# Optimization experiments

Measured on AMD Instinct MI355X. Metric: run time of the kernel, lower is better.

## Reference

```python
import jax, jax.numpy as jnp
import numpy as np
import math

N_FREQS = 32
MARGIN = 0.1
CHOUT = 270
POS_DIM = 2 * N_FREQS ** 2  # 2048


def fourier_emb(positions):
    # positions: [..., 2] in [0, 1]
    width = 1.0 + 2.0 * MARGIN
    p = (positions + MARGIN) / width
    f = jnp.arange(N_FREQS, dtype=p.dtype)
    two_pi = 2.0 * math.pi
    # phase[..., i, j] = 2*pi*(x*i + y*j)  -> flatten to [..., F*F]
    phase = two_pi * (p[..., 0][..., None, None] * f[:, None]
                      + p[..., 1][..., None, None] * f[None, :])
    phase = phase.reshape(*phase.shape[:-2], N_FREQS * N_FREQS)
    return jnp.concatenate([jnp.sin(phase), jnp.cos(phase)], axis=-1)  # [..., 2F^2]


def setup_inputs() -> dict:
    key = jax.random.key(0)
    k1, k2, k3 = jax.random.split(key, 3)
    B, C, T = 32, 273, 3000
    brain_data = jax.random.normal(k1, (B, C, T), dtype=jnp.float32)
    channel_layout = jax.random.uniform(k2, (B, C, 2), dtype=jnp.float32)
    heads = jax.random.normal(k3, (CHOUT, POS_DIM), dtype=jnp.float32) / POS_DIM ** 0.5
    return {"brain_data": brain_data, "channel_layout": channel_layout, "heads": heads}


def reference(brain_data, channel_layout, heads):
    # Eval mode: all channels valid, no dropout mask, zero score offset.
    emb = fourier_emb(channel_layout)                      # [B, C, D]
    scores = jnp.einsum('bcd,od->boc', emb, heads)         # [B, O, C]
    weights = jax.nn.softmax(scores, axis=-1)              # softmax over channels
    out = jnp.einsum('bct,boc->bot', brain_data, weights)  # [B, O, T]
    return out
```

## Files before the change

### kernel.cpp

```cpp
#include <hip/hip_runtime.h>
#include <hip/hip_bf16.h>
#include <hip/hip_fp16.h>

#define NB 32
#define NC 273
#define NT 3000
#define NO 270
#define ND 2048
#define CP 288

typedef _Float16 f16x8 __attribute__((ext_vector_type(8)));
typedef float f32x4 __attribute__((ext_vector_type(4)));

#define S_OFF 55296000UL
#define W_OFF 64730880UL
#define H_OFF 69707520UL

__device__ __forceinline__ unsigned short f2h_bits(float f) {
  _Float16 h = (_Float16)f;
  unsigned short u;
  __builtin_memcpy(&u, &h, 2);
  return u;
}

__global__ void heads_cvt_kernel(const float* __restrict__ heads,
                                 _Float16* __restrict__ hh) {
  const size_t idx = ((size_t)blockIdx.x * 256 + threadIdx.x) * 8;
  const float4 a = *reinterpret_cast<const float4*>(heads + idx);
  const float4 c = *reinterpret_cast<const float4*>(heads + idx + 4);
  f16x8 v;
  v[0] = (_Float16)a.x; v[1] = (_Float16)a.y; v[2] = (_Float16)a.z; v[3] = (_Float16)a.w;
  v[4] = (_Float16)c.x; v[5] = (_Float16)c.y; v[6] = (_Float16)c.z; v[7] = (_Float16)c.w;
  *reinterpret_cast<f16x8*>(hh + idx) = v;
}

__global__ void emb_kernel(const float* __restrict__ layout,
                           _Float16* __restrict__ emb) {
  const int bc = blockIdx.x;
  const float x = layout[2 * bc];
  const float y = layout[2 * bc + 1];
  const float inv = 1.0f / 1.2f;
  const float px = (x + 0.1f) * inv;
  const float py = (y + 0.1f) * inv;
  const float two_pi = 6.283185307179586f;

  const int d0 = threadIdx.x * 8;
  const bool is_sin = d0 < 1024;
  const int dd0 = d0 & 1023;
  const int i = dd0 >> 5;
  const int j = dd0 & 31;
  const float base = px * (float)i + py * (float)j;

  unsigned short h[8];
#pragma unroll
  for (int s = 0; s < 8; ++s) {
    const float ph = two_pi * (base + py * (float)s);
    const float v = is_sin ? sinf(ph) : cosf(ph);
    h[s] = f2h_bits(v);
  }
  uint4 u;
  u.x = (unsigned)h[0] | ((unsigned)h[1] << 16);
  u.y = (unsigned)h[2] | ((unsigned)h[3] << 16);
  u.z = (unsigned)h[4] | ((unsigned)h[5] << 16);
  u.w = (unsigned)h[6] | ((unsigned)h[7] << 16);
  *reinterpret_cast<uint4*>(emb + (size_t)bc * ND + d0) = u;
}

__global__ void scores_kernel(const _Float16* __restrict__ hh,
                              const _Float16* __restrict__ emb,
                              float* __restrict__ scores) {
  __shared__ _Float16 As[64][72];
  __shared__ _Float16 Bs[64][72];
  const int b = blockIdx.z, o0 = blockIdx.y * 64, c0 = blockIdx.x * 64;
  const int tid = threadIdx.x;
  const int lane = tid & 63, w = tid >> 6;
  const int wm = (w >> 1) * 32, wn = (w & 1) * 32;
  const int ln = lane & 15, quad = lane >> 4;
  const int sr = tid >> 2;
  const int sk = (tid & 3) * 16;
  const _Float16* embB = emb + (size_t)b * NC * ND;

  f32x4 acc[2][2] = {};

  for (int k0 = 0; k0 < ND; k0 += 64) {
    {
      const int o = o0 + sr;
      uint4 u0 = {0, 0, 0, 0}, u1 = {0, 0, 0, 0};
      if (o < NO) {
        const uint4* p = reinterpret_cast<const uint4*>(hh + (size_t)o * ND + k0 + sk);
        u0 = p[0]; u1 = p[1];
      }
      *reinterpret_cast<uint4*>(&As[sr][sk]) = u0;
      *reinterpret_cast<uint4*>(&As[sr][sk + 8]) = u1;
    }
    {
      const int c = c0 + sr;
      uint4 u0 = {0, 0, 0, 0}, u1 = {0, 0, 0, 0};
      if (c < NC) {
        const uint4* p = reinterpret_cast<const uint4*>(embB + (size_t)c * ND + k0 + sk);
        u0 = p[0]; u1 = p[1];
      }
      *reinterpret_cast<uint4*>(&Bs[sr][sk]) = u0;
      *reinterpret_cast<uint4*>(&Bs[sr][sk + 8]) = u1;
    }
    __syncthreads();
#pragma unroll
    for (int ks = 0; ks < 64; ks += 32) {
      const int kf = ks + quad * 8;
      const f16x8 a0 = *reinterpret_cast<const f16x8*>(&As[wm + ln][kf]);
      const f16x8 a1 = *reinterpret_cast<const f16x8*>(&As[wm + 16 + ln][kf]);
      const f16x8 b0 = *reinterpret_cast<const f16x8*>(&Bs[wn + ln][kf]);
      const f16x8 b1 = *reinterpret_cast<const f16x8*>(&Bs[wn + 16 + ln][kf]);
      acc[0][0] = __builtin_amdgcn_mfma_f32_16x16x32_f16(a0, b0, acc[0][0], 0, 0, 0);
      acc[0][1] = __builtin_amdgcn_mfma_f32_16x16x32_f16(a0, b1, acc[0][1], 0, 0, 0);
      acc[1][0] = __builtin_amdgcn_mfma_f32_16x16x32_f16(a1, b0, acc[1][0], 0, 0, 0);
      acc[1][1] = __builtin_amdgcn_mfma_f32_16x16x32_f16(a1, b1, acc[1][1], 0, 0, 0);
    }
    __syncthreads();
  }

  float* sB = scores + (size_t)b * NO * NC;
#pragma unroll
  for (int i = 0; i < 2; ++i) {
    const int ob = o0 + wm + 16 * i + quad * 4;
#pragma unroll
    for (int j = 0; j < 2; ++j) {
      const int c = c0 + wn + 16 * j + ln;
      if (c >= NC) continue;
#pragma unroll
      for (int r = 0; r < 4; ++r) {
        const int o = ob + r;
        if (o < NO) sB[(size_t)o * NC + c] = acc[i][j][r];
      }
    }
  }
}

__global__ void softmax_kernel(const float* __restrict__ sc,
                               _Float16* __restrict__ wq) {
  const int row = blockIdx.x * 4 + (threadIdx.x >> 6);
  const int lane = threadIdx.x & 63;
  const float* p = sc + (size_t)row * NC;
  _Float16* q = wq + (size_t)row * CP;
  float v[5];
  float m = -3.0e38f;
#pragma unroll
  for (int k = 0; k < 5; ++k) {
    const int c = lane + k * 64;
    v[k] = (c < NC) ? p[c] : -3.0e38f;
    m = fmaxf(m, v[k]);
  }
#pragma unroll
  for (int off = 32; off > 0; off >>= 1) m = fmaxf(m, __shfl_xor(m, off));
  float s = 0.f;
#pragma unroll
  for (int k = 0; k < 5; ++k) {
    v[k] = expf(v[k] - m);
    s += v[k];
  }
#pragma unroll
  for (int off = 32; off > 0; off >>= 1) s += __shfl_xor(s, off);
  const float r = 1.0f / s;
#pragma unroll
  for (int k = 0; k < 5; ++k) {
    const int c = lane + k * 64;
    if (c < NC) q[c] = (_Float16)(v[k] * r);
    else if (c < CP) q[c] = (_Float16)0.f;
  }
}

__global__ void transpose_kernel(const float* __restrict__ brain,
                                 _Float16* __restrict__ xh) {
  __shared__ float tile[32][33];
  const int b = blockIdx.z;
  const int c0 = blockIdx.y * 32;
  const int t0 = blockIdx.x * 32;
  const int tid = threadIdx.x;
  {
    const int cl = tid >> 3, tl = (tid & 7) * 4;
    const int c = c0 + cl;
    float4 v = {0.f, 0.f, 0.f, 0.f};
    if (c < NC) {
      const int t = t0 + tl;
      const float* p = brain + ((size_t)b * NC + c) * NT + t;
      if (t + 3 < NT) {
        v = *reinterpret_cast<const float4*>(p);
      } else {
        if (t + 0 < NT) v.x = p[0];
        if (t + 1 < NT) v.y = p[1];
        if (t + 2 < NT) v.z = p[2];
        if (t + 3 < NT) v.w = p[3];
      }
    }
    tile[cl][tl + 0] = v.x;
    tile[cl][tl + 1] = v.y;
    tile[cl][tl + 2] = v.z;
    tile[cl][tl + 3] = v.w;
  }
  __syncthreads();
  {
    const int tl = tid >> 3, cl = (tid & 7) * 4;
    const int t = t0 + tl;
    if (t < NT) {
      const unsigned short h0 = f2h_bits(tile[cl + 0][tl]);
      const unsigned short h1 = f2h_bits(tile[cl + 1][tl]);
      const unsigned short h2 = f2h_bits(tile[cl + 2][tl]);
      const unsigned short h3 = f2h_bits(tile[cl + 3][tl]);
      uint2 u;
      u.x = (unsigned)h0 | ((unsigned)h1 << 16);
      u.y = (unsigned)h2 | ((unsigned)h3 << 16);
      *reinterpret_cast<uint2*>(xh + ((size_t)b * NT + t) * CP + c0 + cl) = u;
    }
  }
}

__global__ void out_kernel(const _Float16* __restrict__ wq,
                           const _Float16* __restrict__ xh,
                           float* __restrict__ out) {
  __shared__ _Float16 As[64][40];
  __shared__ _Float16 Bs[128][40];
  const int b = blockIdx.z, o0 = blockIdx.y * 64, t0 = blockIdx.x * 128;
  const int tid = threadIdx.x;
  const int lane = tid & 63, w = tid >> 6;
  const int wm = (w >> 1) * 32, wn = (w & 1) * 64;
  const int ln = lane & 15, quad = lane >> 4;
  const _Float16* Wb = wq + (size_t)b * NO * CP;
  const _Float16* Xb = xh + (size_t)b * NT * CP;

  const int ar = tid >> 2, ak = (tid & 3) * 8;
  const int br = tid >> 1, bk = (tid & 1) * 16;

  f32x4 acc[2][4] = {};

  for (int k0 = 0; k0 < CP; k0 += 32) {
    {
      const int o = o0 + ar;
      uint4 u = {0, 0, 0, 0};
      if (o < NO) u = *reinterpret_cast<const uint4*>(Wb + (size_t)o * CP + k0 + ak);
      *reinterpret_cast<uint4*>(&As[ar][ak]) = u;
    }
    {
      const int t = t0 + br;
      uint4 u0 = {0, 0, 0, 0}, u1 = {0, 0, 0, 0};
      if (t < NT) {
        const uint4* p = reinterpret_cast<const uint4*>(Xb + (size_t)t * CP + k0 + bk);
        u0 = p[0]; u1 = p[1];
      }
      *reinterpret_cast<uint4*>(&Bs[br][bk]) = u0;
      *reinterpret_cast<uint4*>(&Bs[br][bk + 8]) = u1;
    }
    __syncthreads();
    {
      const int kf = quad * 8;
      const f16x8 a0 = *reinterpret_cast<const f16x8*>(&As[wm + ln][kf]);
      const f16x8 a1 = *reinterpret_cast<const f16x8*>(&As[wm + 16 + ln][kf]);
#pragma unroll
      for (int j = 0; j < 4; ++j) {
        const f16x8 bj = *reinterpret_cast<const f16x8*>(&Bs[wn + 16 * j + ln][kf]);
        acc[0][j] = __builtin_amdgcn_mfma_f32_16x16x32_f16(a0, bj, acc[0][j], 0, 0, 0);
        acc[1][j] = __builtin_amdgcn_mfma_f32_16x16x32_f16(a1, bj, acc[1][j], 0, 0, 0);
      }
    }
    __syncthreads();
  }

  float* oB = out + (size_t)b * NO * NT;
#pragma unroll
  for (int i = 0; i < 2; ++i) {
    const int ob = o0 + wm + 16 * i + quad * 4;
#pragma unroll
    for (int j = 0; j < 4; ++j) {
      const int t = t0 + wn + 16 * j + ln;
      if (t >= NT) continue;
#pragma unroll
      for (int r = 0; r < 4; ++r) {
        const int o = ob + r;
        if (o < NO) oB[(size_t)o * NT + t] = acc[i][j][r];
      }
    }
  }
}

extern "C" void kernel_launch(void* const* d_in, const int* in_sizes, int n_in,
                              void* d_out, int out_size, void* d_ws, size_t ws_size,
                              hipStream_t stream) {
  const float* brain = (const float*)d_in[0];
  const float* layout = (const float*)d_in[1];
  const float* heads = (const float*)d_in[2];
  for (int i = 0; i < n_in; ++i) {
    if (in_sizes[i] == NB * NC * NT) brain = (const float*)d_in[i];
    else if (in_sizes[i] == NB * NC * 2) layout = (const float*)d_in[i];
    else if (in_sizes[i] == NO * ND) heads = (const float*)d_in[i];
  }
  float* out = (float*)d_out;

  _Float16* emb = (_Float16*)d_ws;
  _Float16* xh = (_Float16*)d_ws;
  float* scores = (float*)((char*)d_ws + S_OFF);
  _Float16* wq = (_Float16*)((char*)d_ws + W_OFF);
  _Float16* hh = (_Float16*)((char*)d_ws + H_OFF);

  heads_cvt_kernel<<<NO, 256, 0, stream>>>(heads, hh);
  emb_kernel<<<NB * NC, 256, 0, stream>>>(layout, emb);
  scores_kernel<<<dim3(5, 5, NB), 256, 0, stream>>>(hh, emb, scores);
  softmax_kernel<<<(NB * NO) / 4, 256, 0, stream>>>(scores, wq);
  transpose_kernel<<<dim3((NT + 31) / 32, CP / 32, NB), 256, 0, stream>>>(brain, xh);
  out_kernel<<<dim3((NT + 127) / 128, 5, NB), 256, 0, stream>>>(wq, xh, out);
}
```

Baseline: 309.2 us.

## Fuse Fourier embedding into scores GEMM and co-schedule with transpose in one launch

Removes the separate embedding kernel: the scores GEMM now builds the sin/cos Fourier tile in shared memory on the fly, using range-reduced phases and the hardware sin instruction, with cos expressed as a quarter-period shift. The scores GEMM and the brain-data transpose/fp16 conversion are merged into one launch, with blocks split by index, so the small GEMM grid can overlap with the bandwidth-bound transpose. The transpose tile is enlarged to 64x64 with wider vector loads and stores. This avoids writing and re-reading the large fp16 embedding buffer and two launches. In exchange, sin is recomputed for each output-row tile, and the hardware sin may be less accurate.

```diff
diff --git a/kernel.cpp b/kernel.cpp
--- a/kernel.cpp
+++ b/kernel.cpp
@@ -34,103 +34,163 @@
   *reinterpret_cast<f16x8*>(hh + idx) = v;
 }
 
-__global__ void emb_kernel(const float* __restrict__ layout,
-                           _Float16* __restrict__ emb) {
-  const int bc = blockIdx.x;
-  const float x = layout[2 * bc];
-  const float y = layout[2 * bc + 1];
-  const float inv = 1.0f / 1.2f;
-  const float px = (x + 0.1f) * inv;
-  const float py = (y + 0.1f) * inv;
-  const float two_pi = 6.283185307179586f;
-
-  const int d0 = threadIdx.x * 8;
-  const bool is_sin = d0 < 1024;
-  const int dd0 = d0 & 1023;
-  const int i = dd0 >> 5;
-  const int j = dd0 & 31;
-  const float base = px * (float)i + py * (float)j;
-
-  unsigned short h[8];
-#pragma unroll
-  for (int s = 0; s < 8; ++s) {
-    const float ph = two_pi * (base + py * (float)s);
-    const float v = is_sin ? sinf(ph) : cosf(ph);
-    h[s] = f2h_bits(v);
-  }
-  uint4 u;
-  u.x = (unsigned)h[0] | ((unsigned)h[1] << 16);
-  u.y = (unsigned)h[2] | ((unsigned)h[3] << 16);
-  u.z = (unsigned)h[4] | ((unsigned)h[5] << 16);
-  u.w = (unsigned)h[6] | ((unsigned)h[7] << 16);
-  *reinterpret_cast<uint4*>(emb + (size_t)bc * ND + d0) = u;
-}
-
-__global__ void scores_kernel(const _Float16* __restrict__ hh,
-                              const _Float16* __restrict__ emb,
-                              float* __restrict__ scores) {
-  __shared__ _Float16 As[64][72];
-  __shared__ _Float16 Bs[64][72];
-  const int b = blockIdx.z, o0 = blockIdx.y * 64, c0 = blockIdx.x * 64;
+#define SC_BLOCKS 800
+#define TR_TX 47
+#define TR_BLOCKS (TR_TX * 5 * NB)
+
+__global__ void mid_kernel(const _Float16* __restrict__ hh,
+                           const float* __restrict__ layout,
+                           const float* __restrict__ brain,
+                           float* __restrict__ scores,
+                           _Float16* __restrict__ xh) {
+  __shared__ __align__(16) char smem[18432];
+  const int gid = blockIdx.x;
   const int tid = threadIdx.x;
-  const int lane = tid & 63, w = tid >> 6;
-  const int wm = (w >> 1) * 32, wn = (w & 1) * 32;
-  const int ln = lane & 15, quad = lane >> 4;
-  const int sr = tid >> 2;
-  const int sk = (tid & 3) * 16;
-  const _Float16* embB = emb + (size_t)b * NC * ND;
-
-  f32x4 acc[2][2] = {};
-
-  for (int k0 = 0; k0 < ND; k0 += 64) {
-    {
-      const int o = o0 + sr;
-      uint4 u0 = {0, 0, 0, 0}, u1 = {0, 0, 0, 0};
-      if (o < NO) {
-        const uint4* p = reinterpret_cast<const uint4*>(hh + (size_t)o * ND + k0 + sk);
-        u0 = p[0]; u1 = p[1];
-      }
-      *reinterpret_cast<uint4*>(&As[sr][sk]) = u0;
-      *reinterpret_cast<uint4*>(&As[sr][sk + 8]) = u1;
-    }
-    {
-      const int c = c0 + sr;
-      uint4 u0 = {0, 0, 0, 0}, u1 = {0, 0, 0, 0};
+
+  if (gid < SC_BLOCKS) {
+    _Float16 (*As)[72] = reinterpret_cast<_Float16 (*)[72]>(smem);
+    _Float16 (*Bs)[72] = reinterpret_cast<_Float16 (*)[72]>(smem + 9216);
+    const int b = gid / 25;
+    const int rem = gid % 25;
+    const int o0 = (rem / 5) * 64;
+    const int c0 = (rem % 5) * 64;
+    const int lane = tid & 63, w = tid >> 6;
+    const int wm = (w >> 1) * 32, wn = (w & 1) * 32;
+    const int ln = lane & 15, quad = lane >> 4;
+    const int sr = tid >> 2;
+    const int sk = (tid & 3) * 16;
+
+    const int ch = c0 + sr;
+    float px = 0.f, py = 0.f;
+    if (ch < NC) {
+      const float inv = 1.0f / 1.2f;
+      const float* lp = layout + ((size_t)b * NC + ch) * 2;
+      px = (lp[0] + 0.1f) * inv;
+      py = (lp[1] + 0.1f) * inv;
+    }
+
+    f32x4 acc[2][2] = {};
+
+    for (int k0 = 0; k0 < ND; k0 += 64) {
+      {
+        const int o = o0 + sr;
+        uint4 u0 = {0, 0, 0, 0}, u1 = {0, 0, 0, 0};
+        if (o < NO) {
+          const uint4* p = reinterpret_cast<const uint4*>(hh + (size_t)o * ND + k0 + sk);
+          u0 = p[0]; u1 = p[1];
+        }
+        *reinterpret_cast<uint4*>(&As[sr][sk]) = u0;
+        *reinterpret_cast<uint4*>(&As[sr][sk + 8]) = u1;
+      }
+      {
+        const int kg = k0 + sk;
+        const int dd = kg & 1023;
+        const float base = px * (float)(dd >> 5) + py * (float)(dd & 31)
+                         + ((kg < 1024) ? 0.0f : 0.25f);
+        f16x8 h0, h1;
+#pragma unroll
+        for (int s = 0; s < 8; ++s) {
+          float ph = base + py * (float)s;
+          ph -= floorf(ph);
+          h0[s] = (_Float16)__builtin_amdgcn_sinf(ph);
+        }
+#pragma unroll
+        for (int s = 0; s < 8; ++s) {
+          float ph = base + py * (float)(s + 8);
+          ph -= floorf(ph);
+          h1[s] = (_Float16)__builtin_amdgcn_sinf(ph);
+        }
+        *reinterpret_cast<f16x8*>(&Bs[sr][sk]) = h0;
+        *reinterpret_cast<f16x8*>(&Bs[sr][sk + 8]) = h1;
+      }
+      __syncthreads();
+#pragma unroll
+      for (int ks = 0; ks < 64; ks += 32) {
+        const int kf = ks + quad * 8;
+        const f16x8 a0 = *reinterpret_cast<const f16x8*>(&As[wm + ln][kf]);
+        const f16x8 a1 = *reinterpret_cast<const f16x8*>(&As[wm + 16 + ln][kf]);
+        const f16x8 b0 = *reinterpret_cast<const f16x8*>(&Bs[wn + ln][kf]);
+        const f16x8 b1 = *reinterpret_cast<const f16x8*>(&Bs[wn + 16 + ln][kf]);
+        acc[0][0] = __builtin_amdgcn_mfma_f32_16x16x32_f16(a0, b0, acc[0][0], 0, 0, 0);
+        acc[0][1] = __builtin_amdgcn_mfma_f32_16x16x32_f16(a0, b1, acc[0][1], 0, 0, 0);
+        acc[1][0] = __builtin_amdgcn_mfma_f32_16x16x32_f16(a1, b0, acc[1][0], 0, 0, 0);
+        acc[1][1] = __builtin_amdgcn_mfma_f32_16x16x32_f16(a1, b1, acc[1][1], 0, 0, 0);
+      }
+      __syncthreads();
+    }
+
+    float* sB = scores + (size_t)b * NO * NC;
+#pragma unroll
+    for (int i = 0; i < 2; ++i) {
+      const int ob = o0 + wm + 16 * i + quad * 4;
+#pragma unroll
+      for (int j = 0; j < 2; ++j) {
+        const int cc = c0 + wn + 16 * j + ln;
+        if (cc >= NC) continue;
+#pragma unroll
+        for (int r = 0; r < 4; ++r) {
+          const int o = ob + r;
+          if (o < NO) sB[(size_t)o * NC + cc] = acc[i][j][r];
+        }
+      }
+    }
+  } else {
+    float (*tile)[68] = reinterpret_cast<float (*)[68]>(smem);
+    const int id = gid - SC_BLOCKS;
+    const int tx = id % TR_TX;
+    const int r2 = id / TR_TX;
+    const int c0 = (r2 % 5) * 64;
+    const int b = r2 / 5;
+    const int t0 = tx * 64;
+    {
+      const int cl = tid >> 2;
+      const int tl = (tid & 3) * 16;
+      const int c = c0 + cl;
+      const int t = t0 + tl;
+      float4 v0 = {0.f, 0.f, 0.f, 0.f}, v1 = v0, v2 = v0, v3 = v0;
       if (c < NC) {
-        const uint4* p = reinterpret_cast<const uint4*>(embB + (size_t)c * ND + k0 + sk);
-        u0 = p[0]; u1 = p[1];
-      }
-      *reinterpret_cast<uint4*>(&Bs[sr][sk]) = u0;
-      *reinterpret_cast<uint4*>(&Bs[sr][sk + 8]) = u1;
+        const float* p = brain + ((size_t)b * NC + c) * NT + t;
+        if (t + 15 < NT) {
+          v0 = *reinterpret_cast<const float4*>(p + 0);
+          v1 = *reinterpret_cast<const float4*>(p + 4);
+          v2 = *reinterpret_cast<const float4*>(p + 8);
+          v3 = *reinterpret_cast<const float4*>(p + 12);
+        } else {
+          float tmp[16];
+#pragma unroll
+          for (int e = 0; e < 16; ++e) tmp[e] = (t + e < NT) ? p[e] : 0.f;
+          v0.x = tmp[0];  v0.y = tmp[1];  v0.z = tmp[2];  v0.w = tmp[3];
+          v1.x = tmp[4];  v1.y = tmp[5];  v1.z = tmp[6];  v1.w = tmp[7];
+          v2.x = tmp[8];  v2.y = tmp[9];  v2.z = tmp[10]; v2.w = tmp[11];
+          v3.x = tmp[12]; v3.y = tmp[13]; v3.z = tmp[14]; v3.w = tmp[15];
+        }
+      }
+      *reinterpret_cast<float4*>(&tile[cl][tl + 0]) = v0;
+      *reinterpret_cast<float4*>(&tile[cl][tl + 4]) = v1;
+      *reinterpret_cast<float4*>(&tile[cl][tl + 8]) = v2;
+      *reinterpret_cast<float4*>(&tile[cl][tl + 12]) = v3;
     }
     __syncthreads();
-#pragma unroll
-    for (int ks = 0; ks < 64; ks += 32) {
-      const int kf = ks + quad * 8;
-      const f16x8 a0 = *reinterpret_cast<const f16x8*>(&As[wm + ln][kf]);
-      const f16x8 a1 = *reinterpret_cast<const f16x8*>(&As[wm + 16 + ln][kf]);
-      const f16x8 b0 = *reinterpret_cast<const f16x8*>(&Bs[wn + ln][kf]);
-      const f16x8 b1 = *reinterpret_cast<const f16x8*>(&Bs[wn + 16 + ln][kf]);
-      acc[0][0] = __builtin_amdgcn_mfma_f32_16x16x32_f16(a0, b0, acc[0][0], 0, 0, 0);
-      acc[0][1] = __builtin_amdgcn_mfma_f32_16x16x32_f16(a0, b1, acc[0][1], 0, 0, 0);
-      acc[1][0] = __builtin_amdgcn_mfma_f32_16x16x32_f16(a1, b0, acc[1][0], 0, 0, 0);
-      acc[1][1] = __builtin_amdgcn_mfma_f32_16x16x32_f16(a1, b1, acc[1][1], 0, 0, 0);
-    }
-    __syncthreads();
-  }
-
-  float* sB = scores + (size_t)b * NO * NC;
-#pragma unroll
-  for (int i = 0; i < 2; ++i) {
-    const int ob = o0 + wm + 16 * i + quad * 4;
-#pragma unroll
-    for (int j = 0; j < 2; ++j) {
-      const int c = c0 + wn + 16 * j + ln;
-      if (c >= NC) continue;
-#pragma unroll
-      for (int r = 0; r < 4; ++r) {
-        const int o = ob + r;
-        if (o < NO) sB[(size_t)o * NC + c] = acc[i][j][r];
+    {
+      const int tl = tid >> 2;
+      const int cl = (tid & 3) * 16;
+      const int t = t0 + tl;
+      if (t < NT && (c0 + cl) < CP) {
+        unsigned short h[16];
+#pragma unroll
+        for (int s = 0; s < 16; ++s) h[s] = f2h_bits(tile[cl + s][tl]);
+        uint4 u0, u1;
+        u0.x = (unsigned)h[0]  | ((unsigned)h[1] << 16);
+        u0.y = (unsigned)h[2]  | ((unsigned)h[3] << 16);
+        u0.z = (unsigned)h[4]  | ((unsigned)h[5] << 16);
+        u0.w = (unsigned)h[6]  | ((unsigned)h[7] << 16);
+        u1.x = (unsigned)h[8]  | ((unsigned)h[9] << 16);
+        u1.y = (unsigned)h[10] | ((unsigned)h[11] << 16);
+        u1.z = (unsigned)h[12] | ((unsigned)h[13] << 16);
+        u1.w = (unsigned)h[14] | ((unsigned)h[15] << 16);
+        _Float16* q = xh + ((size_t)b * NT + t) * CP + c0 + cl;
+        *reinterpret_cast<uint4*>(q + 0) = u0;
+        *reinterpret_cast<uint4*>(q + 8) = u1;
       }
     }
   }
@@ -166,51 +226,6 @@
     const int c = lane + k * 64;
     if (c < NC) q[c] = (_Float16)(v[k] * r);
     else if (c < CP) q[c] = (_Float16)0.f;
-  }
-}
-
-__global__ void transpose_kernel(const float* __restrict__ brain,
-                                 _Float16* __restrict__ xh) {
-  __shared__ float tile[32][33];
-  const int b = blockIdx.z;
-  const int c0 = blockIdx.y * 32;
-  const int t0 = blockIdx.x * 32;
-  const int tid = threadIdx.x;
-  {
-    const int cl = tid >> 3, tl = (tid & 7) * 4;
-    const int c = c0 + cl;
-    float4 v = {0.f, 0.f, 0.f, 0.f};
-    if (c < NC) {
-      const int t = t0 + tl;
-      const float* p = brain + ((size_t)b * NC + c) * NT + t;
-      if (t + 3 < NT) {
-        v = *reinterpret_cast<const float4*>(p);
-      } else {
-        if (t + 0 < NT) v.x = p[0];
-        if (t + 1 < NT) v.y = p[1];
-        if (t + 2 < NT) v.z = p[2];
-        if (t + 3 < NT) v.w = p[3];
-      }
-    }
-    tile[cl][tl + 0] = v.x;
-    tile[cl][tl + 1] = v.y;
-    tile[cl][tl + 2] = v.z;
-    tile[cl][tl + 3] = v.w;
-  }
-  __syncthreads();
-  {
-    const int tl = tid >> 3, cl = (tid & 7) * 4;
-    const int t = t0 + tl;
-    if (t < NT) {
-      const unsigned short h0 = f2h_bits(tile[cl + 0][tl]);
-      const unsigned short h1 = f2h_bits(tile[cl + 1][tl]);
-      const unsigned short h2 = f2h_bits(tile[cl + 2][tl]);
-      const unsigned short h3 = f2h_bits(tile[cl + 3][tl]);
-      uint2 u;
-      u.x = (unsigned)h0 | ((unsigned)h1 << 16);
-      u.y = (unsigned)h2 | ((unsigned)h3 << 16);
-      *reinterpret_cast<uint2*>(xh + ((size_t)b * NT + t) * CP + c0 + cl) = u;
-    }
   }
 }
 
@@ -294,16 +309,13 @@
   }
   float* out = (float*)d_out;
 
-  _Float16* emb = (_Float16*)d_ws;
   _Float16* xh = (_Float16*)d_ws;
   float* scores = (float*)((char*)d_ws + S_OFF);
   _Float16* wq = (_Float16*)((char*)d_ws + W_OFF);
   _Float16* hh = (_Float16*)((char*)d_ws + H_OFF);
 
   heads_cvt_kernel<<<NO, 256, 0, stream>>>(heads, hh);
-  emb_kernel<<<NB * NC, 256, 0, stream>>>(layout, emb);
-  scores_kernel<<<dim3(5, 5, NB), 256, 0, stream>>>(hh, emb, scores);
+  mid_kernel<<<SC_BLOCKS + TR_BLOCKS, 256, 0, stream>>>(hh, layout, brain, scores, xh);
   softmax_kernel<<<(NB * NO) / 4, 256, 0, stream>>>(scores, wq);
-  transpose_kernel<<<dim3((NT + 31) / 32, CP / 32, NB), 256, 0, stream>>>(brain, xh);
   out_kernel<<<dim3((NT + 127) / 128, 5, NB), 256, 0, stream>>>(wq, xh, out);
 }
```

New measurement: 270.4 us. 1.14x faster.
